# Kernel tuning notes

Measured on AMD Instinct MI355X. Metric: run time of the kernel, lower is better.

The kernel has to match this reference:

```python
import jax, jax.numpy as jnp
import numpy as np

ALPHA = 1.0
BETA = 10.0
MARGIN = 0.5


def setup_inputs() -> dict:
    key = jax.random.key(0)
    k1, k2 = jax.random.split(key)
    emb = jax.random.normal(k1, (4096, 512), dtype=jnp.float32)
    # module docstring: embeddings are L2-normalized
    emb = emb / jnp.linalg.norm(emb, axis=1, keepdims=True)
    labels = jax.random.randint(k2, (4096,), 0, 64, dtype=jnp.int64)
    return {"embeddings": emb, "labels": labels}


def reference(embeddings, labels):
    n = embeddings.shape[0]
    sim = embeddings @ embeddings.T  # [n, n]
    labels_eq = labels[None, :] == labels[:, None]
    eye = jnp.eye(n, dtype=bool)
    pos_mask = labels_eq & ~eye
    neg_mask = ~labels_eq & ~eye

    # masked exp-sums (masked entries contribute 0, matching torch's
    # clone/NEG_INF/zero-out dance without materializing extra copies)
    pos_exp = jnp.where(pos_mask, jnp.exp(-ALPHA * (sim - MARGIN)), 0.0)
    neg_exp = jnp.where(neg_mask, jnp.exp(BETA * (sim - MARGIN)), 0.0)
    pos_term = (1.0 / ALPHA) * jnp.log1p(pos_exp.sum(axis=1))
    neg_term = (1.0 / BETA) * jnp.log1p(neg_exp.sum(axis=1))

    valid = pos_mask.any(axis=1) & neg_mask.any(axis=1)
    n_valid = valid.sum()
    total = jnp.where(valid, pos_term + neg_term, 0.0).sum()
    return jnp.where(n_valid > 0, total / jnp.maximum(n_valid, 1).astype(sim.dtype), 0.0)
```

## Files before the change

kernel.cpp:

```cpp
#include <hip/hip_runtime.h>
#include <hip/hip_bf16.h>

#define N 4096
#define D 512
#define MARGIN 0.5f
#define BETA 10.0f

typedef __attribute__((ext_vector_type(8))) short short8;
typedef __attribute__((ext_vector_type(4))) float floatx4;

__device__ inline unsigned short f2bf(float f) {
    unsigned u = __float_as_uint(f);
    u += 0x7fffu + ((u >> 16) & 1u);
    return (unsigned short)(u >> 16);
}

__global__ __launch_bounds__(256) void convert_bf16_kernel(
        const float4* __restrict__ in, ushort4* __restrict__ out,
        float* __restrict__ sums ) {
    int idx = blockIdx.x * 256 + threadIdx.x;
    if (idx < 2 * N) sums[idx] = 0.f;
    float4 v = in[idx];
    ushort4 o;
    o.x = f2bf(v.x); o.y = f2bf(v.y); o.z = f2bf(v.z); o.w = f2bf(v.w);
    out[idx] = o;
}

__global__ __launch_bounds__(256, 4) void ms_loss_gemm(
        const unsigned short* __restrict__ Ebf,
        const int* __restrict__ labels,
        float* __restrict__ pos_sum,
        float* __restrict__ neg_sum) {
    __shared__ unsigned short Atile[128 * 32];
    __shared__ unsigned short Btile[128 * 32];
    __shared__ int rlab[128];
    __shared__ int clab[128];

    const int tid  = threadIdx.x;
    const int wave = tid >> 6;
    const int lane = tid & 63;
    const int quad = lane >> 4;
    const int lcol = lane & 15;
    const int wrow = wave >> 1;
    const int wcol = wave & 1;
    const int ibase = blockIdx.y * 128;
    const int jbase = blockIdx.x * 128;

    if (tid < 128)       rlab[tid]       = labels[ibase + tid];
    else                 clab[tid - 128] = labels[jbase + tid - 128];

    floatx4 acc[4][4];
#pragma unroll
    for (int mt = 0; mt < 4; ++mt)
#pragma unroll
        for (int nt = 0; nt < 4; ++nt)
            acc[mt][nt] = (floatx4){0.f, 0.f, 0.f, 0.f};

    const char* Eb = (const char*)Ebf;
    char* Ab = (char*)Atile;
    char* Bb = (char*)Btile;
    const int srow = lane >> 2;
    const int sckb = ((lane & 3) ^ ((lane >> 3) & 3)) * 16;
    const int rdsw = ((lcol >> 1) & 3);

    for (int kt = 0; kt < D / 32; ++kt) {
        __syncthreads();
        const int kb = kt * 64;
#pragma unroll
        for (int it = 0; it < 2; ++it) {
            int r    = wave * 16 + it * 64 + srow;
            int ldso = wave * 1024 + it * 4096 + lane * 16;
            const char* ga = Eb + (size_t)(ibase + r) * (D * 2) + kb + sckb;
            const char* gb = Eb + (size_t)(jbase + r) * (D * 2) + kb + sckb;
            __builtin_amdgcn_global_load_lds(
                (const __attribute__((address_space(1))) void*)ga,
                (__attribute__((address_space(3))) void*)(Ab + ldso), 16, 0, 0);
            __builtin_amdgcn_global_load_lds(
                (const __attribute__((address_space(1))) void*)gb,
                (__attribute__((address_space(3))) void*)(Bb + ldso), 16, 0, 0);
        }
        __syncthreads();

        short8 a[4], b[4];
        const int rchunk = (quad ^ rdsw) * 16;
#pragma unroll
        for (int mt = 0; mt < 4; ++mt) {
            int r = wrow * 64 + mt * 16 + lcol;
            a[mt] = *(const short8*)(Ab + r * 64 + rchunk);
        }
#pragma unroll
        for (int nt = 0; nt < 4; ++nt) {
            int c = wcol * 64 + nt * 16 + lcol;
            b[nt] = *(const short8*)(Bb + c * 64 + rchunk);
        }
#pragma unroll
        for (int mt = 0; mt < 4; ++mt)
#pragma unroll
            for (int nt = 0; nt < 4; ++nt)
                acc[mt][nt] = __builtin_amdgcn_mfma_f32_16x16x32_bf16(
                    a[mt], b[nt], acc[mt][nt], 0, 0, 0);
    }

    int ljv[4], gjv[4];
#pragma unroll
    for (int nt = 0; nt < 4; ++nt) {
        int cl = wcol * 64 + nt * 16 + lcol;
        ljv[nt] = clab[cl];
        gjv[nt] = jbase + cl;
    }

#pragma unroll
    for (int mt = 0; mt < 4; ++mt) {
#pragma unroll
        for (int reg = 0; reg < 4; ++reg) {
            int rl = wrow * 64 + mt * 16 + quad * 4 + reg;
            int gi = ibase + rl;
            int li = rlab[rl];
            float p = 0.f, ng = 0.f;
#pragma unroll
            for (int nt = 0; nt < 4; ++nt) {
                float s = acc[mt][nt][reg];
                if (gi != gjv[nt]) {
                    if (li == ljv[nt])
                        p  += __expf(MARGIN - s);
                    else
                        ng += __expf(BETA * (s - MARGIN));
                }
            }
            p  += __shfl_xor(p, 1);   ng += __shfl_xor(ng, 1);
            p  += __shfl_xor(p, 2);   ng += __shfl_xor(ng, 2);
            p  += __shfl_xor(p, 4);   ng += __shfl_xor(ng, 4);
            p  += __shfl_xor(p, 8);   ng += __shfl_xor(ng, 8);
            if (lcol == 0) {
                atomicAdd(&pos_sum[gi], p);
                atomicAdd(&neg_sum[gi], ng);
            }
        }
    }
}

__global__ __launch_bounds__(256) void finalize_kernel(
        const float4* __restrict__ pos4, const float4* __restrict__ neg4,
        float* __restrict__ out) {
    __shared__ float sb[256];
    __shared__ int   sc[256];
    const int tid = threadIdx.x;
    float tot = 0.f;
    int cnt = 0;
#pragma unroll
    for (int it = 0; it < N / 4 / 256; ++it) {
        int i = it * 256 + tid;
        float4 p = pos4[i];
        float4 ng = neg4[i];
        const float* pp = (const float*)&p;
        const float* nn = (const float*)&ng;
#pragma unroll
        for (int j = 0; j < 4; ++j) {
            if (pp[j] > 0.f && nn[j] > 0.f) {
                tot += log1pf(pp[j]) + (1.0f / BETA) * log1pf(nn[j]);
                cnt += 1;
            }
        }
    }
    sb[tid] = tot; sc[tid] = cnt;
    __syncthreads();
    for (int s = 128; s > 0; s >>= 1) {
        if (tid < s) { sb[tid] += sb[tid + s]; sc[tid] += sc[tid + s]; }
        __syncthreads();
    }
    if (tid == 0) out[0] = (sc[0] > 0) ? sb[0] / (float)sc[0] : 0.f;
}

extern "C" void kernel_launch(void* const* d_in, const int* in_sizes, int n_in,
                              void* d_out, int out_size, void* d_ws, size_t ws_size,
                              hipStream_t stream) {
    const float* emb   = (const float*)d_in[0];
    const int* labels  = (const int*)d_in[1];
    float* out         = (float*)d_out;

    char* ws = (char*)d_ws;
    unsigned short* Ebf = (unsigned short*)ws;
    float* pos_sum = (float*)(ws + (size_t)N * D * 2);
    float* neg_sum = pos_sum + N;

    convert_bf16_kernel<<<(N * D / 4) / 256, 256, 0, stream>>>(
        (const float4*)emb, (ushort4*)Ebf, pos_sum);

    dim3 grid(N / 128, N / 128);
    ms_loss_gemm<<<grid, 256, 0, stream>>>(Ebf, labels, pos_sum, neg_sum);

    finalize_kernel<<<1, 256, 0, stream>>>(
        (const float4*)pos_sum, (const float4*)neg_sum, out);
}
```

Before: 99.85 us.

## Exploit Gram matrix symmetry by computing only upper-triangular tiles

Launches only the upper-triangular 128x128 tile pairs of the symmetric similarity matrix (528 blocks instead of 1024). Off-diagonal blocks also reduce their exp terms along columns and add them to the column rows' sums via extra atomics. Diagonal blocks load a single tile and reuse it for both operands. This roughly halves the MFMA and global-load work, at the cost of a serial loop to decode the tile index, more column atomics, and a less even grid.

Result: faster. 93.16 us (-6.7%).

```diff
diff --git a/kernel.cpp b/kernel.cpp
--- a/kernel.cpp
+++ b/kernel.cpp
@@ -36,6 +36,12 @@
     __shared__ int rlab[128];
     __shared__ int clab[128];
 
+    int t = blockIdx.x;
+    int bi = 0;
+    while (t >= (32 - bi)) { t -= (32 - bi); ++bi; }
+    const int bj = bi + t;
+    const bool diag = (bi == bj);
+
     const int tid  = threadIdx.x;
     const int wave = tid >> 6;
     const int lane = tid & 63;
@@ -43,8 +49,8 @@
     const int lcol = lane & 15;
     const int wrow = wave >> 1;
     const int wcol = wave & 1;
-    const int ibase = blockIdx.y * 128;
-    const int jbase = blockIdx.x * 128;
+    const int ibase = bi * 128;
+    const int jbase = bj * 128;
 
     if (tid < 128)       rlab[tid]       = labels[ibase + tid];
     else                 clab[tid - 128] = labels[jbase + tid - 128];
@@ -59,6 +65,7 @@
     const char* Eb = (const char*)Ebf;
     char* Ab = (char*)Atile;
     char* Bb = (char*)Btile;
+    const char* Bread = diag ? Ab : Bb;
     const int srow = lane >> 2;
     const int sckb = ((lane & 3) ^ ((lane >> 3) & 3)) * 16;
     const int rdsw = ((lcol >> 1) & 3);
@@ -71,13 +78,15 @@
             int r    = wave * 16 + it * 64 + srow;
             int ldso = wave * 1024 + it * 4096 + lane * 16;
             const char* ga = Eb + (size_t)(ibase + r) * (D * 2) + kb + sckb;
-            const char* gb = Eb + (size_t)(jbase + r) * (D * 2) + kb + sckb;
             __builtin_amdgcn_global_load_lds(
                 (const __attribute__((address_space(1))) void*)ga,
                 (__attribute__((address_space(3))) void*)(Ab + ldso), 16, 0, 0);
-            __builtin_amdgcn_global_load_lds(
-                (const __attribute__((address_space(1))) void*)gb,
-                (__attribute__((address_space(3))) void*)(Bb + ldso), 16, 0, 0);
+            if (!diag) {
+                const char* gb = Eb + (size_t)(jbase + r) * (D * 2) + kb + sckb;
+                __builtin_amdgcn_global_load_lds(
+                    (const __attribute__((address_space(1))) void*)gb,
+                    (__attribute__((address_space(3))) void*)(Bb + ldso), 16, 0, 0);
+            }
         }
         __syncthreads();
 
@@ -91,7 +100,7 @@
 #pragma unroll
         for (int nt = 0; nt < 4; ++nt) {
             int c = wcol * 64 + nt * 16 + lcol;
-            b[nt] = *(const short8*)(Bb + c * 64 + rchunk);
+            b[nt] = *(const short8*)(Bread + c * 64 + rchunk);
         }
 #pragma unroll
         for (int mt = 0; mt < 4; ++mt)
@@ -108,6 +117,9 @@
         ljv[nt] = clab[cl];
         gjv[nt] = jbase + cl;
     }
+
+    float colp[4] = {0.f, 0.f, 0.f, 0.f};
+    float coln[4] = {0.f, 0.f, 0.f, 0.f};
 
 #pragma unroll
     for (int mt = 0; mt < 4; ++mt) {
@@ -121,10 +133,13 @@
             for (int nt = 0; nt < 4; ++nt) {
                 float s = acc[mt][nt][reg];
                 if (gi != gjv[nt]) {
-                    if (li == ljv[nt])
-                        p  += __expf(MARGIN - s);
-                    else
-                        ng += __expf(BETA * (s - MARGIN));
+                    if (li == ljv[nt]) {
+                        float e = __expf(MARGIN - s);
+                        p += e;  colp[nt] += e;
+                    } else {
+                        float e = __expf(BETA * (s - MARGIN));
+                        ng += e; coln[nt] += e;
+                    }
                 }
             }
             p  += __shfl_xor(p, 1);   ng += __shfl_xor(ng, 1);
@@ -134,6 +149,20 @@
             if (lcol == 0) {
                 atomicAdd(&pos_sum[gi], p);
                 atomicAdd(&neg_sum[gi], ng);
+            }
+        }
+    }
+
+    if (!diag) {
+#pragma unroll
+        for (int nt = 0; nt < 4; ++nt) {
+            float cp = colp[nt], cn = coln[nt];
+            cp += __shfl_xor(cp, 16);  cn += __shfl_xor(cn, 16);
+            cp += __shfl_xor(cp, 32);  cn += __shfl_xor(cn, 32);
+            if (quad == 0) {
+                int gj = gjv[nt];
+                atomicAdd(&pos_sum[gj], cp);
+                atomicAdd(&neg_sum[gj], cn);
             }
         }
     }
@@ -186,8 +215,7 @@
     convert_bf16_kernel<<<(N * D / 4) / 256, 256, 0, stream>>>(
         (const float4*)emb, (ushort4*)Ebf, pos_sum);
 
-    dim3 grid(N / 128, N / 128);
-    ms_loss_gemm<<<grid, 256, 0, stream>>>(Ebf, labels, pos_sum, neg_sum);
+    ms_loss_gemm<<<(32 * 33) / 2, 256, 0, stream>>>(Ebf, labels, pos_sum, neg_sum);
 
     finalize_kernel<<<1, 256, 0, stream>>>(
         (const float4*)pos_sum, (const float4*)neg_sum, out);
```
